# Kernel tuning notes

Hardware: AMD Instinct MI355X
Metric: run time of the kernel (lower is better)

## Reference

```python
import jax, jax.numpy as jnp
import numpy as np

B, N, D, H, E = 4, 2048, 512, 8, 512   # batch, seq, d_model, heads, dpb_embedding
D1 = 2 * D                              # expand_ratio * d_model (multiple of H)
HD = D1 // H                            # head dim for v/u space
GAMMA = 0.999


def _srms(x):
    # SimpleRMSNorm: x / (||x|| * d^-0.5 + eps)
    return x / (jnp.sqrt(jnp.mean(jnp.square(x), axis=-1, keepdims=True)) + 1e-8)


def setup_inputs() -> dict:
    key = jax.random.key(0)
    ks = jax.random.split(key, 10)
    s = 0.02

    def lin(k, i, o):
        kw, kb = jax.random.split(k)
        return (jax.random.normal(kw, (i, o), jnp.float32) * s,
                jax.random.normal(kb, (o,), jnp.float32) * s)

    Wu, bu = lin(ks[0], D, D1)
    Wv, bv = lin(ks[1], D, D1)
    Wo, bo = lin(ks[2], D1, D)
    Wp, bp = lin(ks[3], 1, E)        # DPB pos_proj: scalar position -> dpb_dim
    W1, b1 = lin(ks[4], E, E)
    W2, b2 = lin(ks[5], E, E)
    W3, b3 = lin(ks[6], E, E)
    Wz, bz = lin(ks[7], E, H * HD)   # DPB out: dpb_dim -> h*head_dim
    x = jax.random.normal(ks[8], (B, N, D), jnp.float32)
    return dict(x=x, Wu=Wu, bu=bu, Wv=Wv, bv=bv, Wo=Wo, bo=bo,
                Wp=Wp, bp=bp, W1=W1, b1=b1, W2=W2, b2=b2, W3=W3, b3=b3,
                Wz=Wz, bz=bz)


def reference(x, Wu, bu, Wv, bv, Wo, bo, Wp, bp, W1, b1, W2, b2, W3, b3, Wz, bz):
    shortcut = x                       # token_shift_type=-1, resi_param=False
    xn = _srms(x)                      # pre_norm = SimpleRMSNorm(d_model)
    u = jax.nn.silu(xn @ Wu + bu)      # b n d1
    v = jax.nn.silu(xn @ Wv + bv)      # b n d1
    b, n, _ = x.shape
    v = v.reshape(b, n, H, HD).transpose(0, 2, 1, 3)   # b h n d

    # --- DPB (Rpe MLP) on positions [0, 1, ..., n-1]; row 0 is the zero lag ---
    pos = jnp.arange(0, n, dtype=x.dtype).reshape(n, 1)  # par_type=1
    hcf = pos @ Wp + bp
    for W, bb in ((W1, b1), (W2, b2), (W3, b3)):         # non-residual layers
        hcf = jax.nn.relu(_srms(hcf)) @ W + bb
    coef = jax.nn.relu(_srms(hcf)) @ Wz + bz             # n, h*d
    coef = coef.reshape(n, H, HD).transpose(1, 0, 2)     # h n d
    zero = coef[:, :1]                                   # h 1 d  (lag 0)
    posc = coef[:, 1:]                                   # h n-1 d (lags 1..n-1)

    # fixed exponential decay gamma^i on positive lags (use_decay=True)
    decay = GAMMA ** jnp.arange(1, n, dtype=x.dtype)[None, :, None]
    # causal: negative lags are zero; rfft zero-pads to 2n
    a = jnp.concatenate([zero, decay * posc, zero], axis=1)  # h, n+1, d

    # --- causal Toeplitz matmul as circular conv of length 2n ---
    m = 2 * n
    fv = jnp.fft.rfft(v, m, axis=2)           # b h m/2+1 d
    fa = jnp.fft.rfft(a, m, axis=1)[None]     # 1 h m/2+1 d
    out = jnp.fft.irfft(fv * fa, m, axis=2)[:, :, :n]  # b h n d

    out = out.transpose(0, 2, 1, 3).reshape(b, n, H * HD)  # b n d1
    out = u * out                               # u-gating
    return out @ Wo + bo + shortcut             # output proj + residual
```

## Files before the change

kernel.cpp:

```cpp
#include <hip/hip_runtime.h>
#include <hip/hip_bf16.h>
#include <math.h>

using bf16 = __hip_bfloat16;
typedef short bf16x8 __attribute__((ext_vector_type(8)));
typedef float f32x4 __attribute__((ext_vector_type(4)));

#define GAMMA_LOG2 (-0.0014434688536725045f)

union Bf16Bits { bf16 h; unsigned short s; };
union VecU { uint4 q; unsigned short s[8]; };

__device__ inline unsigned short bf16_bits(float z)
{
    Bf16Bits u;
    u.h = __float2bfloat16(z);
    return u.s;
}

__device__ inline unsigned int packbf2(float a, float b)
{
    return (unsigned int)bf16_bits(a) | ((unsigned int)bf16_bits(b) << 16);
}

__device__ __forceinline__ void async_copy16(unsigned short* lds, const bf16* g)
{
    __builtin_amdgcn_global_load_lds(
        (const __attribute__((address_space(1))) unsigned int*)(const void*)g,
        (__attribute__((address_space(3))) unsigned int*)(void*)lds,
        16, 0, 0);
}

struct PrepArgs {
    const float* src[3];
    bf16* dst[3];
    int R[3];
    int C[3];
    int pfx[4];
};

__global__ void k_prologue(PrepArgs pa,
                           const float* __restrict__ W1, const float* __restrict__ W2,
                           const float* __restrict__ W3, const float* __restrict__ Wz,
                           bf16* __restrict__ Wf,
                           const float* __restrict__ x, bf16* __restrict__ xn)
{
    const int bidg = blockIdx.x;
    if (bidg < 1536) {
        __shared__ float tile[32][33];
        int bid = bidg;
        int seg = 0;
        while (bid >= pa.pfx[seg + 1]) ++seg;
        int local = bid - pa.pfx[seg];
        int R = pa.R[seg], C = pa.C[seg];
        int ctiles = C >> 5;
        int c0 = (local % ctiles) * 32, r0 = (local / ctiles) * 32;
        const float* in = pa.src[seg];
        bf16* out = pa.dst[seg];
        int tx = threadIdx.x & 31, ty = threadIdx.x >> 5;
#pragma unroll
        for (int i = 0; i < 4; ++i) {
            int r = r0 + ty + 8 * i;
            tile[ty + 8 * i][tx] = in[(size_t)r * C + c0 + tx];
        }
        __syncthreads();
#pragma unroll
        for (int i = 0; i < 4; ++i) {
            int cc = c0 + ty + 8 * i, rr = r0 + tx;
            out[(size_t)cc * R + rr] = __float2bfloat16(tile[tx][ty + 8 * i]);
        }
        return;
    }
    if (bidg < 2176) {
        int g = (bidg - 1536) * 256 + threadIdx.x;
        int unit = g >> 15;
        int idx = g & 32767;
        int lane = idx & 63;
        int nj = (idx >> 6) & 7;
        int ks = (idx >> 9) & 15;
        int wc = idx >> 13;
        int lm = lane & 15, lq = lane >> 4;
        int k0 = ks * 32 + lq * 8;
        const float* src;
        int N, o;
        if (unit < 3) {
            src = (unit == 0) ? W1 : (unit == 1) ? W2 : W3;
            N = 512;
            o = wc * 128 + nj * 16 + lm;
        } else {
            src = Wz;
            N = 1024;
            o = (unit - 3) * 512 + wc * 128 + nj * 16 + lm;
        }
        VecU v;
#pragma unroll
        for (int j = 0; j < 8; ++j)
            v.s[j] = bf16_bits(src[(size_t)(k0 + j) * N + o]);
        *(uint4*)(void*)(Wf + (size_t)g * 8) = v.q;
        return;
    }
    {
        int row = bidg - 2176, t = threadIdx.x;
        const float* xr = x + (size_t)row * 512;
        float a = xr[t], b = xr[t + 256];
        float v = a * a + b * b;
#pragma unroll
        for (int m = 32; m >= 1; m >>= 1) v += __shfl_xor(v, m, 64);
        __shared__ float ws[4];
        if ((t & 63) == 0) ws[t >> 6] = v;
        __syncthreads();
        float tot = ws[0] + ws[1] + ws[2] + ws[3];
        float s = 1.f / (sqrtf(tot * (1.f / 512.f)) + 1e-8f);
        bf16* o = xn + (size_t)row * 512;
        o[t] = __float2bfloat16(a * s);
        o[t + 256] = __float2bfloat16(b * s);
    }
}

__global__ void k_gate_transpose(const bf16* __restrict__ ud1t, const bf16* __restrict__ uv,
                                 bf16* __restrict__ out)
{
    __shared__ unsigned short tile[64][65];
    const int b = blockIdx.z;
    const int t = threadIdx.x;
    int c0 = blockIdx.x * 64, t0 = blockIdx.y * 64;
#pragma unroll
    for (int it = 0; it < 2; ++it) {
        int r = it * 32 + (t >> 3), cc = (t & 7) * 8;
        VecU v;
        v.q = *(const uint4*)(const void*)(ud1t + ((size_t)b * 1024 + c0 + r) * 2048 + t0 + cc);
#pragma unroll
        for (int i = 0; i < 8; ++i) tile[r][cc + i] = v.s[i];
    }
    __syncthreads();
#pragma unroll
    for (int it = 0; it < 2; ++it) {
        int tt = it * 32 + (t >> 3), cc = (t & 7) * 8;
        VecU vu;
        vu.q = *(const uint4*)(const void*)(uv + ((size_t)b * 2048 + t0 + tt) * 2048 + c0 + cc);
        VecU vo;
#pragma unroll
        for (int i = 0; i < 8; ++i) {
            Bf16Bits cv, uu;
            cv.s = tile[cc + i][tt];
            uu.s = vu.s[i];
            vo.s[i] = bf16_bits(__bfloat162float(cv.h) * __bfloat162float(uu.h));
        }
        *(uint4*)(void*)(out + ((size_t)b * 2048 + t0 + tt) * 1024 + c0 + cc) = vo.q;
    }
}

struct SharedFused {
    union {
        struct { unsigned short AB[2][2][4096]; } g;
        struct {
            unsigned short X[32][520];
            float sq2[32][33];
            float red[16][32];
            float scale[32];
        } m;
    };
};

__global__ __launch_bounds__(1024, 2) void k_uv_mlp2(
    const bf16* __restrict__ A, const bf16* __restrict__ Bt,
    const float* __restrict__ bu, const float* __restrict__ bv,
    const float* __restrict__ Wp, const float* __restrict__ bp,
    const bf16* __restrict__ Wf,
    const float* __restrict__ b1, const float* __restrict__ b2,
    const float* __restrict__ b3, const float* __restrict__ bz,
    bf16* __restrict__ uvb, bf16* __restrict__ vtb, bf16* __restrict__ atb)
{
    __shared__ SharedFused sh;

    const int tid = threadIdx.x, lane = tid & 63, w = tid >> 6;
    const int lm = lane & 15, lq = lane >> 4;

    if (blockIdx.x < 64) {
        unsigned short (&X)[32][520] = sh.m.X;
        float (&sq2)[32][33] = sh.m.sq2;
        float (&red)[16][32] = sh.m.red;
        float (&scale)[32] = sh.m.scale;
        const int posBase = blockIdx.x * 32;

        {
            const int r = tid >> 5;
            const int cb = tid & 31;
            const int c0 = cb * 16;
            float vals[16];
            float ssq = 0.f;
            const float fp = (float)(posBase + r);
#pragma unroll
            for (int e = 0; e < 16; ++e) {
                float z = fp * Wp[c0 + e] + bp[c0 + e];
                vals[e] = z;
                ssq += z * z;
            }
            sq2[r][cb] = ssq;
            __syncthreads();
            float tot = 0.f;
#pragma unroll
            for (int i = 0; i < 32; ++i) tot += sq2[r][i];
            float s = 1.f / (sqrtf(tot * (1.f / 512.f)) + 1e-8f);
            unsigned int* xrow = (unsigned int*)&X[r][c0];
#pragma unroll
            for (int e = 0; e < 8; ++e)
                xrow[e] = packbf2(fmaxf(vals[2 * e] * s, 0.f), fmaxf(vals[2 * e + 1] * s, 0.f));
            __syncthreads();
        }

        const int wc = w >> 2, njb = (w & 3) * 2;

        auto layer_mm = [&](const bf16* Wu_, f32x4 (&acc)[2][2]) {
            const bf16* base = Wu_ + (size_t)wc * 65536 + (size_t)njb * 512 + (size_t)lane * 8;
            bf16x8 B00, B01, B10, B11, B20, B21, B30, B31;
#define GL2(D0, D1, KS)                                                       \
            asm volatile("global_load_dwordx4 %0, %2, off\n\t"                \
                         "global_load_dwordx4 %1, %2, off offset:1024"        \
                         : "=&v"(D0), "=&v"(D1)                               \
                         : "v"(base + (size_t)(KS) * 4096) : "memory");
#define WAITV(N)                                                              \
            asm volatile("s_waitcnt vmcnt(" #N ")" ::: "memory");             \
            __builtin_amdgcn_sched_barrier(0);
#define MMST(BA, BB, KS) {                                                    \
            bf16x8 af0 = *(const bf16x8*)(const void*)&X[lm][(KS) * 32 + lq * 8]; \
            bf16x8 af1 = *(const bf16x8*)(const void*)&X[16 + lm][(KS) * 32 + lq * 8]; \
            acc[0][0] = __builtin_amdgcn_mfma_f32_16x16x32_bf16(af0, BA, acc[0][0], 0, 0, 0); \
            acc[0][1] = __builtin_amdgcn_mfma_f32_16x16x32_bf16(af0, BB, acc[0][1], 0, 0, 0); \
            acc[1][0] = __builtin_amdgcn_mfma_f32_16x16x32_bf16(af1, BA, acc[1][0], 0, 0, 0); \
            acc[1][1] = __builtin_amdgcn_mfma_f32_16x16x32_bf16(af1, BB, acc[1][1], 0, 0, 0); }
            GL2(B00, B01, 0) GL2(B10, B11, 1) GL2(B20, B21, 2) GL2(B30, B31, 3)
            WAITV(6) MMST(B00, B01, 0)  GL2(B00, B01, 4)
            WAITV(6) MMST(B10, B11, 1)  GL2(B10, B11, 5)
            WAITV(6) MMST(B20, B21, 2)  GL2(B20, B21, 6)
            WAITV(6) MMST(B30, B31, 3)  GL2(B30, B31, 7)
            WAITV(6) MMST(B00, B01, 4)  GL2(B00, B01, 8)
            WAITV(6) MMST(B10, B11, 5)  GL2(B10, B11, 9)
            WAITV(6) MMST(B20, B21, 6)  GL2(B20, B21, 10)
            WAITV(6) MMST(B30, B31, 7)  GL2(B30, B31, 11)
            WAITV(6) MMST(B00, B01, 8)  GL2(B00, B01, 12)
            WAITV(6) MMST(B10, B11, 9)  GL2(B10, B11, 13)
            WAITV(6) MMST(B20, B21, 10) GL2(B20, B21, 14)
            WAITV(6) MMST(B30, B31, 11) GL2(B30, B31, 15)
            WAITV(6) MMST(B00, B01, 12)
            WAITV(4) MMST(B10, B11, 13)
            WAITV(2) MMST(B20, B21, 14)
            WAITV(0) MMST(B30, B31, 15)
#undef GL2
#undef WAITV
#undef MMST
        };

        const float* bs[3] = {b1, b2, b3};
        for (int l = 0; l < 3; ++l) {
            f32x4 acc[2][2];
#pragma unroll
            for (int mi = 0; mi < 2; ++mi)
#pragma unroll
                for (int i = 0; i < 2; ++i) acc[mi][i] = (f32x4){0.f, 0.f, 0.f, 0.f};
            layer_mm(Wf + (size_t)l * 262144, acc);
#pragma unroll
            for (int mi = 0; mi < 2; ++mi)
#pragma unroll
                for (int nj = 0; nj < 2; ++nj) {
                    float bb = bs[l][w * 32 + nj * 16 + lm];
#pragma unroll
                    for (int r = 0; r < 4; ++r) acc[mi][nj][r] += bb;
                }
            float pr[2][4] = {{0.f, 0.f, 0.f, 0.f}, {0.f, 0.f, 0.f, 0.f}};
#pragma unroll
            for (int mi = 0; mi < 2; ++mi)
#pragma unroll
                for (int nj = 0; nj < 2; ++nj)
#pragma unroll
                    for (int r = 0; r < 4; ++r) pr[mi][r] += acc[mi][nj][r] * acc[mi][nj][r];
#pragma unroll
            for (int m = 1; m < 16; m <<= 1)
#pragma unroll
                for (int mi = 0; mi < 2; ++mi)
#pragma unroll
                    for (int r = 0; r < 4; ++r) pr[mi][r] += __shfl_xor(pr[mi][r], m);
            if (lm == 0)
#pragma unroll
                for (int mi = 0; mi < 2; ++mi)
#pragma unroll
                    for (int r = 0; r < 4; ++r) red[w][mi * 16 + lq * 4 + r] = pr[mi][r];
            __syncthreads();
            if (tid < 32) {
                float tot = 0.f;
#pragma unroll
                for (int wv = 0; wv < 16; ++wv) tot += red[wv][tid];
                scale[tid] = 1.f / (sqrtf(tot * (1.f / 512.f)) + 1e-8f);
            }
            __syncthreads();
#pragma unroll
            for (int mi = 0; mi < 2; ++mi)
#pragma unroll
                for (int nj = 0; nj < 2; ++nj) {
                    int col = w * 32 + nj * 16 + lm;
#pragma unroll
                    for (int r = 0; r < 4; ++r) {
                        int row = mi * 16 + lq * 4 + r;
                        float z = fmaxf(acc[mi][nj][r] * scale[row], 0.f);
                        *(unsigned short*)&X[row][col] = bf16_bits(z);
                    }
                }
            __syncthreads();
        }

#pragma unroll
        for (int h = 0; h < 2; ++h) {
            f32x4 acc[2][2];
#pragma unroll
            for (int mi = 0; mi < 2; ++mi)
#pragma unroll
                for (int i = 0; i < 2; ++i) acc[mi][i] = (f32x4){0.f, 0.f, 0.f, 0.f};
            layer_mm(Wf + (size_t)(3 + h) * 262144, acc);
#pragma unroll
            for (int mi = 0; mi < 2; ++mi)
#pragma unroll
                for (int nj = 0; nj < 2; ++nj) {
                    int col = h * 512 + w * 32 + nj * 16 + lm;
                    float bb = bz[col];
                    int pos0 = posBase + mi * 16 + lq * 4;
                    float zs[4];
#pragma unroll
                    for (int r = 0; r < 4; ++r)
                        zs[r] = (acc[mi][nj][r] + bb) * exp2f((float)(pos0 + r) * GAMMA_LOG2);
                    uint2 o;
                    o.x = packbf2(zs[0], zs[1]);
                    o.y = packbf2(zs[2], zs[3]);
                    *(uint2*)(void*)(atb + (size_t)col * 2048 + pos0) = o;
                }
        }
        return;
    }

    unsigned short (&AB)[2][2][4096] = sh.g.AB;

    const int gid = (int)blockIdx.x - 64;
    const int wm = (w >> 2) * 32, wn = (w & 3) * 32;
    const long rowBase = (long)(gid & 63) * 128, colBase = (long)(gid >> 6) * 128;

    const int isB = tid >> 9;
    const int ci  = tid & 511;
    const int srow = ci >> 2;
    const int sqz  = (ci & 3) ^ ((srow >> 1) & 3);
    const bf16* gsrc = (isB ? (Bt + (colBase + srow) * 512)
                            : (A  + (rowBase + srow) * 512)) + sqz * 8;
    unsigned short* ld0 = &AB[0][isB][(w & 7) * 512];
    unsigned short* ld1 = &AB[1][isB][(w & 7) * 512];

    const int rdA = ((wm + lm) * 4 + (lq ^ ((lm >> 1) & 3))) * 8;
    const int rdB = ((wn + lm) * 4 + (lq ^ ((lm >> 1) & 3))) * 8;

    f32x4 acc[2][2];
    f32x4 zz = {0.f, 0.f, 0.f, 0.f};
#pragma unroll
    for (int i = 0; i < 2; ++i)
#pragma unroll
        for (int j = 0; j < 2; ++j) acc[i][j] = zz;

    async_copy16(ld0, gsrc);
    __syncthreads();

#pragma unroll
    for (int t = 0; t < 16; ++t) {
        const int cur = t & 1;
        if (t < 15)
            async_copy16(cur ? ld0 : ld1, gsrc + (t + 1) * 32);
        bf16x8 af[2], bfr[2];
#pragma unroll
        for (int mi = 0; mi < 2; ++mi)
            af[mi] = *(const bf16x8*)(const void*)&AB[cur][0][rdA + mi * 512];
#pragma unroll
        for (int nj = 0; nj < 2; ++nj)
            bfr[nj] = *(const bf16x8*)(const void*)&AB[cur][1][rdB + nj * 512];
#pragma unroll
        for (int mi = 0; mi < 2; ++mi)
#pragma unroll
            for (int nj = 0; nj < 2; ++nj)
                acc[mi][nj] = __builtin_amdgcn_mfma_f32_16x16x32_bf16(af[mi], bfr[nj], acc[mi][nj], 0, 0, 0);
        if (t < 15) __syncthreads();
    }

    const bool vhalf = colBase >= 1024;
    if (!vhalf) {
#pragma unroll
        for (int mi = 0; mi < 2; ++mi)
#pragma unroll
            for (int nj = 0; nj < 2; ++nj) {
                long col = colBase + wn + nj * 16 + lm;
                float bb = bu[col];
                long row0 = rowBase + wm + mi * 16 + lq * 4;
#pragma unroll
                for (int r = 0; r < 4; ++r) {
                    float z = acc[mi][nj][r] + bb;
                    z = z / (1.f + __expf(-z));
                    uvb[(size_t)(row0 + r) * 2048 + col] = __float2bfloat16(z);
                }
            }
    } else {
        __syncthreads();
        unsigned short* shv = &AB[0][0][0];
#pragma unroll
        for (int mi = 0; mi < 2; ++mi)
#pragma unroll
            for (int nj = 0; nj < 2; ++nj) {
                int c_local = wn + nj * 16 + lm;
                float bb = bv[colBase - 1024 + c_local];
                int t_local = wm + mi * 16 + lq * 4;
                float zs[4];
#pragma unroll
                for (int r = 0; r < 4; ++r) {
                    float z = acc[mi][nj][r] + bb;
                    zs[r] = z / (1.f + __expf(-z));
                }
                int p = (t_local + 8 * c_local) & 127;
                uint2 o;
                o.x = packbf2(zs[0], zs[1]);
                o.y = packbf2(zs[2], zs[3]);
                *(uint2*)(void*)&shv[c_local * 128 + p] = o;
            }
        __syncthreads();
        const int b   = (int)(rowBase >> 11);
        const int tb0 = (int)(rowBase & 2047);
        const long cb = colBase - 1024;
        const int cl = tid >> 4;
        const int ch = tid & 15;
#pragma unroll
        for (int it = 0; it < 2; ++it) {
            int c_local = it * 64 + cl;
            int p = (ch * 8 + 8 * c_local) & 127;
            uint4 q = *(const uint4*)(const void*)&shv[c_local * 128 + p];
            *(uint4*)(void*)(vtb + ((size_t)b * 1024 + cb + c_local) * 2048 + tb0 + ch * 8) = q;
        }
    }
}

__global__ __launch_bounds__(256, 4) void k_gemm_out2(
    const bf16* __restrict__ A, const bf16* __restrict__ Bt,
    const float* __restrict__ bias0, const float* __restrict__ addsrc,
    float* __restrict__ outp)
{
    __shared__ unsigned short As[2][64 * 32];
    __shared__ unsigned short Bs[2][128 * 32];

    const int tid = threadIdx.x, lane = tid & 63, w = tid >> 6;
    const int lm = lane & 15, lq = lane >> 4;
    const int wm = (w >> 1) * 32, wn = (w & 1) * 64;
    const long rowBase = (long)blockIdx.x * 64, colBase = (long)blockIdx.y * 128;

    const int srow = tid >> 2;
    const int sqz  = (tid & 3) ^ ((srow >> 1) & 3);
    const bf16* gA  = A  + (rowBase + srow) * 1024 + sqz * 8;
    const bf16* gB  = Bt + (colBase + srow) * 1024 + sqz * 8;
    const bf16* gB2 = gB + (size_t)64 * 1024;
    const int lsA = w * 512;
    const int lsB0 = w * 512, lsB1 = 2048 + w * 512;

    const int rdA = ((wm + lm) * 4 + (lq ^ ((lm >> 1) & 3))) * 8;
    const int rdB = ((wn + lm) * 4 + (lq ^ ((lm >> 1) & 3))) * 8;

    f32x4 acc[2][4];
    f32x4 zz = {0.f, 0.f, 0.f, 0.f};
#pragma unroll
    for (int i = 0; i < 2; ++i)
#pragma unroll
        for (int j = 0; j < 4; ++j) acc[i][j] = zz;

    async_copy16(&As[0][lsA], gA);
    async_copy16(&Bs[0][lsB0], gB);
    async_copy16(&Bs[0][lsB1], gB2);
    __syncthreads();

#pragma unroll
    for (int t = 0; t < 32; ++t) {
        const int cur = t & 1;
        if (t < 31) {
            const int kk = (t + 1) * 32;
            async_copy16(&As[cur ^ 1][lsA], gA + kk);
            async_copy16(&Bs[cur ^ 1][lsB0], gB + kk);
            async_copy16(&Bs[cur ^ 1][lsB1], gB2 + kk);
        }
        bf16x8 af[2], bfr[4];
#pragma unroll
        for (int mi = 0; mi < 2; ++mi)
            af[mi] = *(const bf16x8*)(const void*)&As[cur][rdA + mi * 512];
#pragma unroll
        for (int nj = 0; nj < 4; ++nj)
            bfr[nj] = *(const bf16x8*)(const void*)&Bs[cur][rdB + nj * 512];
#pragma unroll
        for (int mi = 0; mi < 2; ++mi)
#pragma unroll
            for (int nj = 0; nj < 4; ++nj)
                acc[mi][nj] = __builtin_amdgcn_mfma_f32_16x16x32_bf16(af[mi], bfr[nj], acc[mi][nj], 0, 0, 0);
        if (t < 31) __syncthreads();
    }

#pragma unroll
    for (int mi = 0; mi < 2; ++mi)
#pragma unroll
        for (int nj = 0; nj < 4; ++nj) {
            long col = colBase + wn + nj * 16 + lm;
            float bb = bias0[col];
#pragma unroll
            for (int r = 0; r < 4; ++r) {
                long row = rowBase + wm + mi * 16 + lq * 4 + r;
                size_t off = (size_t)row * 512 + col;
                outp[off] = acc[mi][nj][r] + bb + addsrc[off];
            }
        }
}

__global__ __launch_bounds__(256, 4) void k_conv_mfma(
    const bf16* __restrict__ vt, const bf16* __restrict__ at, bf16* __restrict__ ud1t)
{
    __shared__ unsigned short ash2[2][2068];
    __shared__ unsigned short vsh[4][3072];

    const int tid = threadIdx.x, lane = tid & 63, w = tid >> 6;
    const int c = blockIdx.x;

    {
        const unsigned short* asrc = (const unsigned short*)(at + (size_t)c * 2048);
        for (int i = tid; i < 2068; i += 256) {
#pragma unroll
            for (int k = 0; k < 2; ++k) {
                int src = 2047 - i - k;
                ash2[k][i] = (src >= 0) ? asrc[src] : (unsigned short)0;
            }
        }
    }
    {
        const bf16* vsrc = vt + ((size_t)w * 1024 + c) * 2048;
#pragma unroll
        for (int q = 0; q < 4; ++q) {
            int li = q * 64 + lane;
            int tile = li >> 1, hf = li & 1;
            *(uint4*)(void*)&vsh[w][tile * 24 + hf * 8] =
                *(const uint4*)(const void*)(vsrc + li * 8);
        }
    }
    __syncthreads();

    const int lm = lane & 15, lq = lane >> 4;
    const int h = lq >> 1, p0 = (lq & 1) * 8;
    const int kcopy = (lm + 1) & 1;
    const int base = 31 - 16 * h - lm + p0 - kcopy;
    const unsigned int* aw = (const unsigned int*)(void*)&ash2[kcopy][0] + (base >> 1);
    const unsigned short* vw = &vsh[w][0];

    f32x4 acc[8];
    f32x4 zz = {0.f, 0.f, 0.f, 0.f};
#pragma unroll
    for (int i = 0; i < 8; ++i) acc[i] = zz;
    const bf16x8 zfrag = (bf16x8)(short)0;

    for (int d2 = 0; d2 < 16; d2 += 2) {
        bf16x8 vf[8];
        const int tb = lm - d2 - h;
        {
            int T = tb > 0 ? tb : 0;
            bf16x8 f = *(const bf16x8*)(const void*)(vw + T * 24 + p0);
            vf[0] = (tb < 0) ? zfrag : f;
        }
#pragma unroll
        for (int dl = 1; dl < 8; ++dl)
            vf[dl] = *(const bf16x8*)(const void*)(vw + (dl * 16 + tb) * 24 + p0);

#pragma unroll
        for (int dt = 0; dt < 8; ++dt) {
            const int m16 = (63 - ((dt * 16 + d2) >> 1)) * 16;
            union { unsigned int u[4]; bf16x8 v; } af;
            af.u[0] = aw[m16 + 0];
            af.u[1] = aw[m16 + 1];
            af.u[2] = aw[m16 + 2];
            af.u[3] = aw[m16 + 3];
#pragma unroll
            for (int dl = 0; dl < 8 - dt; ++dl)
                acc[dt + dl] = __builtin_amdgcn_mfma_f32_16x16x32_bf16(af.v, vf[dl], acc[dt + dl], 0, 0, 0);
        }
    }

    __syncthreads();
    float* stg = (float*)(void*)((char*)(void*)&ash2[0][0] + w * 1024);
    bf16* dst = ud1t + ((size_t)w * 1024 + c) * 2048;
#pragma unroll
    for (int jg = 0; jg < 8; ++jg) {
        *(f32x4*)(void*)&stg[lm * 16 + lq * 4] = acc[jg];
        f32x4 vv = *(const f32x4*)(const void*)&stg[lane * 4];
        uint2 o;
        o.x = packbf2(vv.x, vv.y);
        o.y = packbf2(vv.z, vv.w);
        *(uint2*)(void*)(dst + jg * 256 + lane * 4) = o;
    }
}

extern "C" void kernel_launch(void* const* d_in, const int* in_sizes, int n_in,
                              void* d_out, int out_size, void* d_ws, size_t ws_size,
                              hipStream_t stream)
{
    const float* x  = (const float*)d_in[0];
    const float* Wu = (const float*)d_in[1];
    const float* bu = (const float*)d_in[2];
    const float* Wv = (const float*)d_in[3];
    const float* bv = (const float*)d_in[4];
    const float* Wo = (const float*)d_in[5];
    const float* bo = (const float*)d_in[6];
    const float* Wp = (const float*)d_in[7];
    const float* bp = (const float*)d_in[8];
    const float* W1 = (const float*)d_in[9];
    const float* b1 = (const float*)d_in[10];
    const float* W2 = (const float*)d_in[11];
    const float* b2 = (const float*)d_in[12];
    const float* W3 = (const float*)d_in[13];
    const float* b3 = (const float*)d_in[14];
    const float* Wz = (const float*)d_in[15];
    const float* bz = (const float*)d_in[16];

    char* p = (char*)d_ws;
    auto carve = [&](size_t bytes) { void* q = (void*)p; p += (bytes + 255) & ~(size_t)255; return q; };
    bf16*  xn   = (bf16*)carve((size_t)8192 * 512 * 2);
    bf16*  Wuvt = (bf16*)carve((size_t)2048 * 512 * 2);
    bf16*  Wot  = (bf16*)carve((size_t)512 * 1024 * 2);
    bf16*  Wf   = (bf16*)carve((size_t)5 * 262144 * 2);
    bf16*  uvb  = (bf16*)carve((size_t)8192 * 2048 * 2);
    bf16*  ud1  = (bf16*)carve((size_t)8192 * 1024 * 2);
    bf16*  vtb  = (bf16*)carve((size_t)4 * 1024 * 2048 * 2);
    bf16*  atb  = (bf16*)carve((size_t)1024 * 2048 * 2);
    bf16*  ud1t = (bf16*)carve((size_t)4 * 1024 * 2048 * 2);

    PrepArgs pa;
    const float* srcs[3] = {Wu, Wv, Wo};
    bf16* dsts[3] = {Wuvt, Wuvt + (size_t)1024 * 512, Wot};
    int Rs[3] = {512, 512, 1024};
    int Cs[3] = {1024, 1024, 512};
    int acc_t = 0;
    for (int i = 0; i < 3; ++i) {
        pa.src[i] = srcs[i]; pa.dst[i] = dsts[i]; pa.R[i] = Rs[i]; pa.C[i] = Cs[i];
        pa.pfx[i] = acc_t;
        acc_t += (Rs[i] / 32) * (Cs[i] / 32);
    }
    pa.pfx[3] = acc_t;
    k_prologue<<<1536 + 640 + 8192, 256, 0, stream>>>(pa, W1, W2, W3, Wz, Wf, x, xn);

    k_uv_mlp2<<<1088, 1024, 0, stream>>>(xn, Wuvt, bu, bv, Wp, bp,
                                         Wf, b1, b2, b3, bz, uvb, vtb, atb);

    k_conv_mfma<<<dim3(1024), 256, 0, stream>>>(vtb, atb, ud1t);

    k_gate_transpose<<<dim3(16, 32, 4), 256, 0, stream>>>(ud1t, uvb, ud1);

    k_gemm_out2<<<dim3(128, 4), 256, 0, stream>>>(ud1, Wot, bo, x, (float*)d_out);
}
```

Baseline: 207.8 us.

## Fuse u-gating into conv epilogue, store u transposed, drop gate-transpose kernel

The u projection is now written in the same channel-major transposed layout as v, so the conv kernel's epilogue can multiply by u directly. This removes the separate gate-transpose kernel and its round trip of the full activation tensor. The output GEMM now reads the transposed gated result and transposes it into LDS with scalar stores, in place of the earlier async copies. That adds LDS write work and synchronous global loads in the GEMM main loop.

```diff
diff --git a/kernel.cpp b/kernel.cpp
--- a/kernel.cpp
+++ b/kernel.cpp
@@ -21,6 +21,13 @@
 __device__ inline unsigned int packbf2(float a, float b)
 {
     return (unsigned int)bf16_bits(a) | ((unsigned int)bf16_bits(b) << 16);
+}
+
+__device__ inline float bfs2f(unsigned short s)
+{
+    Bf16Bits u;
+    u.s = s;
+    return __bfloat162float(u.h);
 }
 
 __device__ __forceinline__ void async_copy16(unsigned short* lds, const bf16* g)
@@ -117,39 +124,6 @@
     }
 }
 
-__global__ void k_gate_transpose(const bf16* __restrict__ ud1t, const bf16* __restrict__ uv,
-                                 bf16* __restrict__ out)
-{
-    __shared__ unsigned short tile[64][65];
-    const int b = blockIdx.z;
-    const int t = threadIdx.x;
-    int c0 = blockIdx.x * 64, t0 = blockIdx.y * 64;
-#pragma unroll
-    for (int it = 0; it < 2; ++it) {
-        int r = it * 32 + (t >> 3), cc = (t & 7) * 8;
-        VecU v;
-        v.q = *(const uint4*)(const void*)(ud1t + ((size_t)b * 1024 + c0 + r) * 2048 + t0 + cc);
-#pragma unroll
-        for (int i = 0; i < 8; ++i) tile[r][cc + i] = v.s[i];
-    }
-    __syncthreads();
-#pragma unroll
-    for (int it = 0; it < 2; ++it) {
-        int tt = it * 32 + (t >> 3), cc = (t & 7) * 8;
-        VecU vu;
-        vu.q = *(const uint4*)(const void*)(uv + ((size_t)b * 2048 + t0 + tt) * 2048 + c0 + cc);
-        VecU vo;
-#pragma unroll
-        for (int i = 0; i < 8; ++i) {
-            Bf16Bits cv, uu;
-            cv.s = tile[cc + i][tt];
-            uu.s = vu.s[i];
-            vo.s[i] = bf16_bits(__bfloat162float(cv.h) * __bfloat162float(uu.h));
-        }
-        *(uint4*)(void*)(out + ((size_t)b * 2048 + t0 + tt) * 1024 + c0 + cc) = vo.q;
-    }
-}
-
 struct SharedFused {
     union {
         struct { unsigned short AB[2][2][4096]; } g;
@@ -169,7 +143,7 @@
     const bf16* __restrict__ Wf,
     const float* __restrict__ b1, const float* __restrict__ b2,
     const float* __restrict__ b3, const float* __restrict__ bz,
-    bf16* __restrict__ uvb, bf16* __restrict__ vtb, bf16* __restrict__ atb)
+    bf16* __restrict__ utb, bf16* __restrict__ vtb, bf16* __restrict__ atb)
 {
     __shared__ SharedFused sh;
 
@@ -385,47 +359,35 @@
     }
 
     const bool vhalf = colBase >= 1024;
-    if (!vhalf) {
-#pragma unroll
-        for (int mi = 0; mi < 2; ++mi)
-#pragma unroll
-            for (int nj = 0; nj < 2; ++nj) {
-                long col = colBase + wn + nj * 16 + lm;
-                float bb = bu[col];
-                long row0 = rowBase + wm + mi * 16 + lq * 4;
-#pragma unroll
-                for (int r = 0; r < 4; ++r) {
-                    float z = acc[mi][nj][r] + bb;
-                    z = z / (1.f + __expf(-z));
-                    uvb[(size_t)(row0 + r) * 2048 + col] = __float2bfloat16(z);
-                }
+    bf16* dstT = vhalf ? vtb : utb;
+    const long cbase = vhalf ? (colBase - 1024) : colBase;
+    const float* bb_src = vhalf ? (bv + cbase) : (bu + cbase);
+
+    __syncthreads();
+    unsigned short* shv = &AB[0][0][0];
+#pragma unroll
+    for (int mi = 0; mi < 2; ++mi)
+#pragma unroll
+        for (int nj = 0; nj < 2; ++nj) {
+            int c_local = wn + nj * 16 + lm;
+            float bb = bb_src[c_local];
+            int t_local = wm + mi * 16 + lq * 4;
+            float zs[4];
+#pragma unroll
+            for (int r = 0; r < 4; ++r) {
+                float z = acc[mi][nj][r] + bb;
+                zs[r] = z / (1.f + __expf(-z));
             }
-    } else {
-        __syncthreads();
-        unsigned short* shv = &AB[0][0][0];
-#pragma unroll
-        for (int mi = 0; mi < 2; ++mi)
-#pragma unroll
-            for (int nj = 0; nj < 2; ++nj) {
-                int c_local = wn + nj * 16 + lm;
-                float bb = bv[colBase - 1024 + c_local];
-                int t_local = wm + mi * 16 + lq * 4;
-                float zs[4];
-#pragma unroll
-                for (int r = 0; r < 4; ++r) {
-                    float z = acc[mi][nj][r] + bb;
-                    zs[r] = z / (1.f + __expf(-z));
-                }
-                int p = (t_local + 8 * c_local) & 127;
-                uint2 o;
-                o.x = packbf2(zs[0], zs[1]);
-                o.y = packbf2(zs[2], zs[3]);
-                *(uint2*)(void*)&shv[c_local * 128 + p] = o;
-            }
-        __syncthreads();
+            int p = (t_local + 8 * c_local) & 127;
+            uint2 o;
+            o.x = packbf2(zs[0], zs[1]);
+            o.y = packbf2(zs[2], zs[3]);
+            *(uint2*)(void*)&shv[c_local * 128 + p] = o;
+        }
+    __syncthreads();
+    {
         const int b   = (int)(rowBase >> 11);
         const int tb0 = (int)(rowBase & 2047);
-        const long cb = colBase - 1024;
         const int cl = tid >> 4;
         const int ch = tid & 15;
 #pragma unroll
@@ -433,33 +395,36 @@
             int c_local = it * 64 + cl;
             int p = (ch * 8 + 8 * c_local) & 127;
             uint4 q = *(const uint4*)(const void*)&shv[c_local * 128 + p];
-            *(uint4*)(void*)(vtb + ((size_t)b * 1024 + cb + c_local) * 2048 + tb0 + ch * 8) = q;
+            *(uint4*)(void*)(dstT + ((size_t)b * 1024 + cbase + c_local) * 2048 + tb0 + ch * 8) = q;
         }
     }
 }
 
 __global__ __launch_bounds__(256, 4) void k_gemm_out2(
-    const bf16* __restrict__ A, const bf16* __restrict__ Bt,
+    const bf16* __restrict__ At, const bf16* __restrict__ Bt,
     const float* __restrict__ bias0, const float* __restrict__ addsrc,
     float* __restrict__ outp)
 {
-    __shared__ unsigned short As[2][64 * 32];
+    __shared__ unsigned short As2[2][64 * 40];
     __shared__ unsigned short Bs[2][128 * 32];
 
     const int tid = threadIdx.x, lane = tid & 63, w = tid >> 6;
     const int lm = lane & 15, lq = lane >> 4;
     const int wm = (w >> 1) * 32, wn = (w & 1) * 64;
     const long rowBase = (long)blockIdx.x * 64, colBase = (long)blockIdx.y * 128;
+    const int bb = (int)(rowBase >> 11);
+    const int t0 = (int)(rowBase & 2047);
 
     const int srow = tid >> 2;
     const int sqz  = (tid & 3) ^ ((srow >> 1) & 3);
-    const bf16* gA  = A  + (rowBase + srow) * 1024 + sqz * 8;
     const bf16* gB  = Bt + (colBase + srow) * 1024 + sqz * 8;
     const bf16* gB2 = gB + (size_t)64 * 1024;
-    const int lsA = w * 512;
-    const int lsB0 = w * 512, lsB1 = 2048 + w * 512;
-
-    const int rdA = ((wm + lm) * 4 + (lq ^ ((lm >> 1) & 3))) * 8;
+    const int lsB0 = (tid >> 6) * 512, lsB1 = 2048 + (tid >> 6) * 512;
+
+    const int sc  = tid >> 3;
+    const int soct = tid & 7;
+    const bf16* gA = At + ((size_t)bb * 1024 + sc) * 2048 + t0 + soct * 8;
+
     const int rdB = ((wn + lm) * 4 + (lq ^ ((lm >> 1) & 3))) * 8;
 
     f32x4 acc[2][4];
@@ -469,7 +434,13 @@
 #pragma unroll
         for (int j = 0; j < 4; ++j) acc[i][j] = zz;
 
-    async_copy16(&As[0][lsA], gA);
+    {
+        VecU q;
+        q.q = *(const uint4*)(const void*)gA;
+#pragma unroll
+        for (int j = 0; j < 8; ++j)
+            As2[0][(soct * 8 + j) * 40 + sc] = q.s[j];
+    }
     async_copy16(&Bs[0][lsB0], gB);
     async_copy16(&Bs[0][lsB1], gB2);
     __syncthreads();
@@ -479,14 +450,18 @@
         const int cur = t & 1;
         if (t < 31) {
             const int kk = (t + 1) * 32;
-            async_copy16(&As[cur ^ 1][lsA], gA + kk);
+            VecU q;
+            q.q = *(const uint4*)(const void*)(gA + (size_t)kk * 2048);
+#pragma unroll
+            for (int j = 0; j < 8; ++j)
+                As2[cur ^ 1][(soct * 8 + j) * 40 + sc] = q.s[j];
             async_copy16(&Bs[cur ^ 1][lsB0], gB + kk);
             async_copy16(&Bs[cur ^ 1][lsB1], gB2 + kk);
         }
         bf16x8 af[2], bfr[4];
 #pragma unroll
         for (int mi = 0; mi < 2; ++mi)
-            af[mi] = *(const bf16x8*)(const void*)&As[cur][rdA + mi * 512];
+            af[mi] = *(const bf16x8*)(const void*)&As2[cur][(wm + mi * 16 + lm) * 40 + lq * 8];
 #pragma unroll
         for (int nj = 0; nj < 4; ++nj)
             bfr[nj] = *(const bf16x8*)(const void*)&Bs[cur][rdB + nj * 512];
@@ -503,18 +478,19 @@
 #pragma unroll
         for (int nj = 0; nj < 4; ++nj) {
             long col = colBase + wn + nj * 16 + lm;
-            float bb = bias0[col];
+            float bbv = bias0[col];
 #pragma unroll
             for (int r = 0; r < 4; ++r) {
                 long row = rowBase + wm + mi * 16 + lq * 4 + r;
                 size_t off = (size_t)row * 512 + col;
-                outp[off] = acc[mi][nj][r] + bb + addsrc[off];
+                outp[off] = acc[mi][nj][r] + bbv + addsrc[off];
             }
         }
 }
 
 __global__ __launch_bounds__(256, 4) void k_conv_mfma(
-    const bf16* __restrict__ vt, const bf16* __restrict__ at, bf16* __restrict__ ud1t)
+    const bf16* __restrict__ vt, const bf16* __restrict__ at,
+    const bf16* __restrict__ ut, bf16* __restrict__ ud1t)
 {
     __shared__ unsigned short ash2[2][2068];
     __shared__ unsigned short vsh[4][3072];
@@ -585,14 +561,18 @@
 
     __syncthreads();
     float* stg = (float*)(void*)((char*)(void*)&ash2[0][0] + w * 1024);
+    const bf16* usrc = ut + ((size_t)w * 1024 + c) * 2048;
     bf16* dst = ud1t + ((size_t)w * 1024 + c) * 2048;
 #pragma unroll
     for (int jg = 0; jg < 8; ++jg) {
         *(f32x4*)(void*)&stg[lm * 16 + lq * 4] = acc[jg];
         f32x4 vv = *(const f32x4*)(const void*)&stg[lane * 4];
+        uint2 uu = *(const uint2*)(const void*)(usrc + jg * 256 + lane * 4);
         uint2 o;
-        o.x = packbf2(vv.x, vv.y);
-        o.y = packbf2(vv.z, vv.w);
+        o.x = packbf2(vv.x * bfs2f((unsigned short)(uu.x & 0xffff)),
+                      vv.y * bfs2f((unsigned short)(uu.x >> 16)));
+        o.y = packbf2(vv.z * bfs2f((unsigned short)(uu.y & 0xffff)),
+                      vv.w * bfs2f((unsigned short)(uu.y >> 16)));
         *(uint2*)(void*)(dst + jg * 256 + lane * 4) = o;
     }
 }
@@ -625,8 +605,7 @@
     bf16*  Wuvt = (bf16*)carve((size_t)2048 * 512 * 2);
     bf16*  Wot  = (bf16*)carve((size_t)512 * 1024 * 2);
     bf16*  Wf   = (bf16*)carve((size_t)5 * 262144 * 2);
-    bf16*  uvb  = (bf16*)carve((size_t)8192 * 2048 * 2);
-    bf16*  ud1  = (bf16*)carve((size_t)8192 * 1024 * 2);
+    bf16*  utb  = (bf16*)carve((size_t)4 * 1024 * 2048 * 2);
     bf16*  vtb  = (bf16*)carve((size_t)4 * 1024 * 2048 * 2);
     bf16*  atb  = (bf16*)carve((size_t)1024 * 2048 * 2);
     bf16*  ud1t = (bf16*)carve((size_t)4 * 1024 * 2048 * 2);
@@ -646,11 +625,9 @@
     k_prologue<<<1536 + 640 + 8192, 256, 0, stream>>>(pa, W1, W2, W3, Wz, Wf, x, xn);
 
     k_uv_mlp2<<<1088, 1024, 0, stream>>>(xn, Wuvt, bu, bv, Wp, bp,
-                                         Wf, b1, b2, b3, bz, uvb, vtb, atb);
-
-    k_conv_mfma<<<dim3(1024), 256, 0, stream>>>(vtb, atb, ud1t);
-
-    k_gate_transpose<<<dim3(16, 32, 4), 256, 0, stream>>>(ud1t, uvb, ud1);
-
-    k_gemm_out2<<<dim3(128, 4), 256, 0, stream>>>(ud1, Wot, bo, x, (float*)d_out);
-}
+                                         Wf, b1, b2, b3, bz, utb, vtb, atb);
+
+    k_conv_mfma<<<dim3(1024), 256, 0, stream>>>(vtb, atb, utb, ud1t);
+
+    k_gemm_out2<<<dim3(128, 4), 256, 0, stream>>>(ud1t, Wot, bo, x, (float*)d_out);
+}
```

Result: slower. 224.3 us (+8.0%).
